# Kernel tuning notes

Hardware: AMD Instinct MI355X
Metric: run time of the kernel (lower is better)

The kernel has to match this reference:

```python
import jax, jax.numpy as jnp
import numpy as np

B, T, DIM, H = 2, 2048, 1024, 16
HD = DIM // H


def setup_inputs() -> dict:
    key = jax.random.key(0)
    k1, k2, k3 = jax.random.split(key, 3)
    std = 1.0 / np.sqrt(DIM)
    x = jax.random.normal(k1, (B, T, DIM), dtype=jnp.float32)
    # torch Linear(dim, 3*dim).weight is [3*dim, dim]; we store the transposed
    # [dim, 3*dim] layout so forward is x @ W_qkv (same math).
    W_qkv = jax.random.uniform(k2, (DIM, 3 * DIM), dtype=jnp.float32, minval=-std, maxval=std)
    W_proj = jax.random.uniform(k3, (DIM, DIM), dtype=jnp.float32, minval=-std, maxval=std)
    return {"x": x, "W_qkv": W_qkv, "W_proj": W_proj}


def reference(x, W_qkv, W_proj):
    Bv, Tv, C = x.shape
    # qkv projection -> [B, T, 3, H, HD] -> q,k,v each [B, H, T, HD]
    qkv = (x @ W_qkv).reshape(Bv, Tv, 3, H, HD)
    qkv = jnp.transpose(qkv, (2, 0, 3, 1, 4))
    q, k, v = qkv[0], qkv[1], qkv[2]
    scale = jnp.asarray(np.sqrt(HD), dtype=x.dtype)
    scores = jnp.einsum('bhqd,bhkd->bhqk', q, k) / scale
    causal = jnp.tril(jnp.ones((Tv, Tv), dtype=bool))  # [T, T]
    scores = jnp.where(causal[None, None, :, :], scores, -jnp.inf)
    attn = jax.nn.softmax(scores, axis=-1)  # [B, H, T, T]
    # entropy per query position, averaged over heads -> [B, T]
    entropy = -(attn * jnp.log(attn + 1e-9)).sum(axis=-1).mean(axis=1)
    # dropout is identity in eval mode
    out = jnp.einsum('bhqk,bhkd->bhqd', attn, v)
    out = jnp.transpose(out, (0, 2, 1, 3)).reshape(Bv, Tv, C)
    return out @ W_proj, entropy
```

## Files before the change

### kernel.cpp

```cpp
#include <hip/hip_runtime.h>


typedef unsigned short u16;
typedef __attribute__((ext_vector_type(8))) __bf16 bf16x8;
typedef __attribute__((ext_vector_type(4))) float float4v;

#define BQ 2
#define TQ 2048
#define DIMQ 1024
#define HQ 16
#define HDQ 64

__device__ __forceinline__ float4v mfma16(bf16x8 a, bf16x8 b, float4v c) {
    return __builtin_amdgcn_mfma_f32_16x16x32_bf16(a, b, c, 0, 0, 0);
}

__device__ __forceinline__ u16 f2bf(float f) {
    unsigned x = __float_as_uint(f);
    return (u16)((x + 0x7FFFu + ((x >> 16) & 1u)) >> 16);
}

__device__ __forceinline__ uint4 cvt8(float4 a, float4 b) {
    union { uint4 v; u16 u[8]; } r;
    r.u[0] = f2bf(a.x); r.u[1] = f2bf(a.y); r.u[2] = f2bf(a.z); r.u[3] = f2bf(a.w);
    r.u[4] = f2bf(b.x); r.u[5] = f2bf(b.y); r.u[6] = f2bf(b.z); r.u[7] = f2bf(b.w);
    return r.v;
}

__device__ __forceinline__ void async16(const u16* g, u16* l) {
    __builtin_amdgcn_global_load_lds(
        (const __attribute__((address_space(1))) void*)g,
        (__attribute__((address_space(3))) void*)l, 16, 0, 0);
}

__device__ __forceinline__ void plswap(unsigned& a, unsigned& b) {
    asm("v_permlane32_swap_b32 %0, %1" : "+v"(a), "+v"(b));
    asm("v_permlane16_swap_b32 %0, %1" : "+v"(a), "+v"(b));
}

__device__ __forceinline__ void tr_tile(
    const float* __restrict__ in, u16* __restrict__ out, int R, int C,
    int tx, int ty, int tid, float (*T)[68])
{
    const int k0 = ty * 64, n0 = tx * 64;
    {
        int r = tid >> 2, cc = (tid & 3) << 4;
        const float* src = in + (size_t)(k0 + r) * C + n0 + cc;
        float4 v0 = ((const float4*)src)[0];
        float4 v1 = ((const float4*)src)[1];
        float4 v2 = ((const float4*)src)[2];
        float4 v3 = ((const float4*)src)[3];
        *(float4*)&T[r][cc + 0]  = v0;
        *(float4*)&T[r][cc + 4]  = v1;
        *(float4*)&T[r][cc + 8]  = v2;
        *(float4*)&T[r][cc + 12] = v3;
    }
    __syncthreads();
    {
        int nr = tid >> 2, kc = (tid & 3) << 4;
        union { uint4 v; u16 u[8]; } o0, o1;
#pragma unroll
        for (int j = 0; j < 8; ++j) o0.u[j] = f2bf(T[kc + j][nr]);
#pragma unroll
        for (int j = 0; j < 8; ++j) o1.u[j] = f2bf(T[kc + 8 + j][nr]);
        u16* dst = out + (size_t)(n0 + nr) * R + k0 + kc;
        ((uint4*)dst)[0] = o0.v;
        *(uint4*)(dst + 8) = o1.v;
    }
}

__global__ __launch_bounds__(256) void prep_kernel(
    const float* __restrict__ x, const float* __restrict__ Wq,
    const float* __restrict__ Wp,
    u16* __restrict__ xb, u16* __restrict__ Wt, u16* __restrict__ Wpt)
{
    __shared__ float T[64][68];
    const int bx = blockIdx.x, tid = threadIdx.x;
    if (bx < 2048) {
        int i = (bx * 256 + tid) * 8;
        float4 a = *(const float4*)(x + i);
        float4 b = *(const float4*)(x + i + 4);
        *(uint4*)(xb + i) = cvt8(a, b);
    } else if (bx < 2816) {
        int bb = bx - 2048;
        tr_tile(Wq, Wt, DIMQ, 3 * DIMQ, bb % 48, bb / 48, tid, T);
    } else {
        int bb = bx - 2816;
        tr_tile(Wp, Wpt, DIMQ, DIMQ, bb & 15, bb >> 4, tid, T);
    }
}

__global__ __launch_bounds__(256) void tr_cvt(
    const float* __restrict__ in, u16* __restrict__ out, int R, int C)
{
    __shared__ float T[64][68];
    tr_tile(in, out, R, C, blockIdx.x, blockIdx.y, threadIdx.x, T);
}

template <int TILEM, int MODE>
__global__ __launch_bounds__(256) void gemm_db(
    const u16* __restrict__ A, const u16* __restrict__ Bt,
    int M, int N, int K,
    u16* __restrict__ Qo, u16* __restrict__ Ko, u16* __restrict__ Vt,
    float* __restrict__ Of, const float* __restrict__ EntIn)
{
    constexpr int MT = TILEM / 32;
    constexpr int AR = TILEM / 64;
    __shared__ u16 As[2][TILEM * 32];
    __shared__ u16 Bs[2][128 * 32];

    const int tid = threadIdx.x;
    const int nbn = gridDim.x;
    const int flat = blockIdx.y * nbn + blockIdx.x;
    const int cpx = (nbn * gridDim.y) >> 3;
    const int swz = (flat & 7) * cpx + (flat >> 3);
    const int bm = swz / nbn, bn = swz % nbn;
    const int wave = tid >> 6, lane = tid & 63;
    const int quad = lane >> 4, c = lane & 15;
    const int wm = wave >> 1, wn = wave & 1;
    const int x3 = c & 3;

    const float4v z = {0.f, 0.f, 0.f, 0.f};
    float4v acc[MT][4];
#pragma unroll
    for (int mt = 0; mt < MT; ++mt)
#pragma unroll
        for (int tn = 0; tn < 4; ++tn) acc[mt][tn] = z;

    const int srow = tid >> 2;
    const int schunk8 = (((tid & 3) ^ (srow & 3)) << 3);
    const u16* ga = A  + (size_t)(bm * TILEM + srow) * K + schunk8;
    const u16* gb = Bt + (size_t)(bn * 128  + srow) * K + schunk8;

#pragma unroll
    for (int p = 0; p < AR; ++p)
        async16(ga + (size_t)(p * 64) * K, As[0] + p * 2048 + tid * 8);
#pragma unroll
    for (int p = 0; p < 2; ++p)
        async16(gb + (size_t)(p * 64) * K, Bs[0] + p * 2048 + tid * 8);

    const int niter = K >> 5;
    for (int it = 0; it < niter; ++it) {
        __syncthreads();
        if (it + 1 < niter) {
            const int nb = (it + 1) & 1;
            const int kc = (it + 1) * 32;
#pragma unroll
            for (int p = 0; p < AR; ++p)
                async16(ga + kc + (size_t)(p * 64) * K, As[nb] + p * 2048 + tid * 8);
#pragma unroll
            for (int p = 0; p < 2; ++p)
                async16(gb + kc + (size_t)(p * 64) * K, Bs[nb] + p * 2048 + tid * 8);
        }
        const u16* as = As[it & 1];
        const u16* bs = Bs[it & 1];

        bf16x8 af[MT], bfr[4];
#pragma unroll
        for (int mt = 0; mt < MT; ++mt)
            af[mt] = *(const bf16x8*)&as[(wm * (TILEM / 2) + mt * 16 + c) * 32 +
                                         ((quad ^ x3) << 3)];
#pragma unroll
        for (int tn = 0; tn < 4; ++tn)
            bfr[tn] = *(const bf16x8*)&bs[(wn * 64 + tn * 16 + c) * 32 +
                                          ((quad ^ x3) << 3)];
#pragma unroll
        for (int mt = 0; mt < MT; ++mt)
#pragma unroll
            for (int tn = 0; tn < 4; ++tn)
                acc[mt][tn] = mfma16(af[mt], bfr[tn], acc[mt][tn]);
    }

#pragma unroll
    for (int mt = 0; mt < MT; ++mt)
#pragma unroll
        for (int tn = 0; tn < 4; ++tn) {
            int gm0 = bm * TILEM + wm * (TILEM / 2) + mt * 16 + quad * 4;
            int gn  = bn * 128 + wn * 64 + tn * 16 + c;
            if (MODE == 0) {
                int s = gn >> 10, h = (gn >> 6) & 15, d = gn & 63;
                int b = gm0 >> 11, t0 = gm0 & 2047;
                size_t bh = (size_t)(b * HQ + h);
                if (s == 2) {
                    union { unsigned long long w; u16 u[4]; } pk;
#pragma unroll
                    for (int r = 0; r < 4; ++r) pk.u[r] = f2bf(acc[mt][tn][r]);
                    *(unsigned long long*)&Vt[(bh * HDQ + d) * TQ + t0] = pk.w;
                } else {
                    u16* dst = (s == 0) ? Qo : Ko;
                    float sc = (s == 0) ? 0.18033688f : 1.0f;
#pragma unroll
                    for (int r = 0; r < 4; ++r)
                        dst[(bh * TQ + t0 + r) * HDQ + d] = f2bf(acc[mt][tn][r] * sc);
                }
            } else {
#pragma unroll
                for (int r = 0; r < 4; ++r)
                    Of[(size_t)(gm0 + r) * N + gn] = acc[mt][tn][r];
            }
        }

    if (MODE == 1 && bn == 0 && bm < 16) {
        int i = bm * 256 + tid;
        int b = i >> 11, t = i & 2047;
        float s = 0.f;
#pragma unroll
        for (int h = 0; h < HQ; ++h) s += EntIn[((size_t)(b * HQ + h)) * TQ + t];
        Of[(size_t)BQ * TQ * DIMQ + i] = s * (1.0f / HQ);
    }
}

__global__ __launch_bounds__(256) void attn_kernel(
    const u16* __restrict__ Q, const u16* __restrict__ K,
    const u16* __restrict__ Vt, u16* __restrict__ AO,
    float* __restrict__ Ent)
{
    const int d = blockIdx.x;
    const int j = d >> 3;
    const int bh = (d & 7) * 4 + (j >> 4);
    int pt = j & 15;
    if (j & 32) pt = 15 - pt;
    const int qt[2] = { pt, 31 - pt };

    const int tid = threadIdx.x;
    const int wave = tid >> 6, lane = tid & 63;
    const int kw = wave & 1;
    const int qh = wave >> 1;
    const int quad = lane >> 4, c = lane & 15;
    const int x7 = c & 7;

    __shared__ u16 Ks[2][64 * 64];
    __shared__ u16 Vs[2][64 * 64];
    __shared__ float Red[2][64][64];
    __shared__ float lred[2][2][2][16], tred[2][2][2][16];

    const u16* Qp = Q  + (size_t)bh * TQ * HDQ;
    const u16* Kp = K  + (size_t)bh * TQ * HDQ;
    const u16* Vp = Vt + (size_t)bh * HDQ * TQ;

    const int qb[2] = { qt[0] * 64 + qh * 32, qt[1] * 64 + qh * 32 };

    bf16x8 qf[2][2][2];
#pragma unroll
    for (int s = 0; s < 2; ++s)
#pragma unroll
        for (int qs = 0; qs < 2; ++qs) {
            const u16* qr = Qp + (size_t)(qb[s] + qs * 16 + c) * HDQ;
            qf[s][qs][0] = *(const bf16x8*)(qr + quad * 8);
            qf[s][qs][1] = *(const bf16x8*)(qr + 32 + quad * 8);
        }

    const float MX2 = 17.312336f;
    const float4v z = {0.f, 0.f, 0.f, 0.f};
    const float4v mz = {-MX2, -MX2, -MX2, -MX2};
    float4v oacc[2][2][4];
#pragma unroll
    for (int s = 0; s < 2; ++s)
#pragma unroll
        for (int qs = 0; qs < 2; ++qs)
#pragma unroll
            for (int tn = 0; tn < 4; ++tn) oacc[s][qs][tn] = z;
    float lp[2][2] = {{0.f,0.f},{0.f,0.f}}, tp[2][2] = {{0.f,0.f},{0.f,0.f}};

    const int ntile = qt[1] + 1;

    const int srow = tid >> 3;
    const int schunk8 = (((tid & 7) ^ (srow & 7)) << 3);
    const u16* ka = Kp + (size_t)srow * HDQ + schunk8;
    const u16* va = Vp + (size_t)srow * TQ + schunk8;

    {
        async16(ka, Ks[0] + tid * 8);
        async16(ka + (size_t)32 * HDQ, Ks[0] + 2048 + tid * 8);
        async16(va, Vs[0] + tid * 8);
        async16(va + (size_t)32 * TQ, Vs[0] + 2048 + tid * 8);
    }

    for (int jt = 0; jt < ntile; ++jt) {
        __syncthreads();
        if (jt + 1 < ntile) {
            int nb = (jt + 1) & 1;
            async16(ka + (size_t)((jt + 1) * 64) * HDQ, Ks[nb] + tid * 8);
            async16(ka + (size_t)((jt + 1) * 64 + 32) * HDQ, Ks[nb] + 2048 + tid * 8);
            async16(va + (jt + 1) * 64, Vs[nb] + tid * 8);
            async16(va + (size_t)32 * TQ + (jt + 1) * 64, Vs[nb] + 2048 + tid * 8);
        }
        const u16* ksb = Ks[jt & 1];
        const u16* vsb = Vs[jt & 1];

        bf16x8 kf[2][2], vf[4];
#pragma unroll
        for (int kt = 0; kt < 2; ++kt) {
            int base = (kw * 32 + kt * 16 + c) * 64;
            kf[kt][0] = *(const bf16x8*)&ksb[base + ((quad ^ x7) << 3)];
            kf[kt][1] = *(const bf16x8*)&ksb[base + (((quad + 4) ^ x7) << 3)];
        }
#pragma unroll
        for (int tn = 0; tn < 4; ++tn)
            vf[tn] = *(const bf16x8*)&vsb[(tn * 16 + c) * 64 +
                                          (((kw * 4 + quad) ^ x7) << 3)];

#pragma unroll
        for (int s = 0; s < 2; ++s) {
            if (s == 0 && jt > qt[0]) continue;
#pragma unroll
            for (int qs = 0; qs < 2; ++qs) {
                unsigned w0[2], w1[2];
#pragma unroll
                for (int kt = 0; kt < 2; ++kt) {
                    float4v sacc = mz;
                    sacc = mfma16(kf[kt][0], qf[s][qs][0], sacc);
                    sacc = mfma16(kf[kt][1], qf[s][qs][1], sacc);
                    if (jt == qt[s]) {
#pragma unroll
                        for (int r = 0; r < 4; ++r) {
                            int kg = jt * 64 + kw * 32 + kt * 16 + quad * 4 + r;
                            if (kg > qb[s] + qs * 16 + c) sacc[r] = -1e30f;
                        }
                    }
                    float pv[4];
#pragma unroll
                    for (int r = 0; r < 4; ++r) {
                        float sv = sacc[r];
                        float p;
                        asm("v_exp_f32 %0, %1" : "=v"(p) : "v"(sv));
                        lp[s][qs] += p;
                        tp[s][qs] += p * sv;
                        pv[r] = p;
                    }
                    asm("v_cvt_pk_bf16_f32 %0, %1, %2"
                        : "=v"(w0[kt]) : "v"(pv[0]), "v"(pv[1]));
                    asm("v_cvt_pk_bf16_f32 %0, %1, %2"
                        : "=v"(w1[kt]) : "v"(pv[2]), "v"(pv[3]));
                }
                plswap(w0[0], w0[1]);
                plswap(w1[0], w1[1]);
                union { uint4 u; bf16x8 v; } P;
                P.u = (uint4){w0[0], w1[0], w0[1], w1[1]};
                __builtin_amdgcn_s_setprio(1);
#pragma unroll
                for (int tn = 0; tn < 4; ++tn)
                    oacc[s][qs][tn] = mfma16(vf[tn], P.v, oacc[s][qs][tn]);
                __builtin_amdgcn_s_setprio(0);
            }
        }
    }

    __syncthreads();
#pragma unroll
    for (int s = 0; s < 2; ++s)
#pragma unroll
        for (int qs = 0; qs < 2; ++qs) {
            lp[s][qs] += __shfl_xor(lp[s][qs], 16);
            lp[s][qs] += __shfl_xor(lp[s][qs], 32);
            tp[s][qs] += __shfl_xor(tp[s][qs], 16);
            tp[s][qs] += __shfl_xor(tp[s][qs], 32);
        }

    if (kw == 1) {
#pragma unroll
        for (int s = 0; s < 2; ++s)
#pragma unroll
            for (int qs = 0; qs < 2; ++qs) {
#pragma unroll
                for (int tn = 0; tn < 4; ++tn)
#pragma unroll
                    for (int r = 0; r < 4; ++r)
                        Red[qh][((s * 2 + qs) * 4 + tn) * 4 + r][lane] =
                            oacc[s][qs][tn][r];
                if (quad == 0) {
                    lred[qh][s][qs][c] = lp[s][qs];
                    tred[qh][s][qs][c] = tp[s][qs];
                }
            }
    }
    __syncthreads();
    if (kw == 0) {
        const int b = bh >> 4, h = bh & 15;
#pragma unroll
        for (int s = 0; s < 2; ++s)
#pragma unroll
            for (int qs = 0; qs < 2; ++qs) {
#pragma unroll
                for (int tn = 0; tn < 4; ++tn)
#pragma unroll
                    for (int r = 0; r < 4; ++r)
                        oacc[s][qs][tn][r] +=
                            Red[qh][((s * 2 + qs) * 4 + tn) * 4 + r][lane];
                float l = lp[s][qs] + lred[qh][s][qs][c];
                float t = tp[s][qs] + tred[qh][s][qs][c];

                float inv = 1.0f / l;
                u16* dst = AO + ((size_t)(b * TQ + qb[s] + qs * 16 + c)) * DIMQ
                           + h * HDQ;
#pragma unroll
                for (int tn = 0; tn < 4; ++tn) {
                    unsigned u[4];
#pragma unroll
                    for (int r = 0; r < 4; ++r)
                        u[r] = (unsigned)f2bf(oacc[s][qs][tn][r] * inv);
                    uint2 pk;
                    pk.x = u[0] | (u[1] << 16);
                    pk.y = u[2] | (u[3] << 16);
                    *(uint2*)(dst + tn * 16 + quad * 4) = pk;
                }
                if (quad == 0)
                    Ent[(size_t)bh * TQ + qb[s] + qs * 16 + c] =
                        __logf(l) - 0.69314718f * t / l;
            }
    }
}

extern "C" void kernel_launch(void* const* d_in, const int* in_sizes, int n_in,
                              void* d_out, int out_size, void* d_ws, size_t ws_size,
                              hipStream_t stream) {
    const float* x     = (const float*)d_in[0];
    const float* Wqkv  = (const float*)d_in[1];
    const float* Wproj = (const float*)d_in[2];
    float* out = (float*)d_out;

    const size_t NE = (size_t)BQ * HQ * TQ * HDQ;
    const size_t WQN = (size_t)3 * DIMQ * DIMQ;
    const size_t WPN = (size_t)DIMQ * DIMQ;
    u16* Qb  = (u16*)d_ws;
    u16* Kb  = Qb + NE;
    u16* Vtb = Kb + NE;
    u16* xb  = Vtb + NE;
    u16* Wt  = xb + NE;
    u16* AO  = xb;

    const size_t need = (4 * NE + WQN + WPN) * 2 + (size_t)BQ * HQ * TQ * 4;
    const bool room = ws_size >= need;
    u16* Wpt = room ? (Wt + WQN) : Wt;
    float* Ent = room ? (float*)(Wpt + WPN) : (float*)(Wt + WQN);

    prep_kernel<<<dim3(room ? 3072 : 2816), 256, 0, stream>>>(
        x, Wqkv, Wproj, xb, Wt, Wpt);
    gemm_db<128, 0><<<dim3(24, 32), 256, 0, stream>>>(
        xb, Wt, BQ * TQ, 3 * DIMQ, DIMQ, Qb, Kb, Vtb, nullptr, nullptr);
    if (!room)
        tr_cvt<<<dim3(16, 16), 256, 0, stream>>>(Wproj, Wpt, DIMQ, DIMQ);
    attn_kernel<<<dim3(512), 256, 0, stream>>>(Qb, Kb, Vtb, AO, Ent);
    gemm_db<64, 1><<<dim3(8, 64), 256, 0, stream>>>(
        AO, Wpt, BQ * TQ, DIMQ, DIMQ, nullptr, nullptr, nullptr, out, Ent);
}
```

Baseline: 177.9 us.

## Double attention block to 512 threads with one 16-row query slice per wave

The attention kernel now uses 8 waves per block, with each wave handling a single 16-row query slice instead of two, halving per-wave accumulator and Q-fragment registers. The block's shared memory is consolidated into one K/V double buffer, which is reused for the cross-wave output reduction, so the block needs less shared memory. Launch bounds request 512 threads with 4 blocks per CU to raise occupancy. In exchange, each K/V fragment read from shared memory is amortized over fewer MFMAs, and the register cap may force spills.

Result: faster. 168.2 us, median of 3 (-5.5%).

```diff
diff --git a/kernel.cpp b/kernel.cpp
--- a/kernel.cpp
+++ b/kernel.cpp
@@ -210,7 +210,7 @@
     }
 }
 
-__global__ __launch_bounds__(256) void attn_kernel(
+__global__ __launch_bounds__(512, 4) void attn_kernel(
     const u16* __restrict__ Q, const u16* __restrict__ K,
     const u16* __restrict__ Vt, u16* __restrict__ AO,
     float* __restrict__ Ent)
@@ -229,38 +229,32 @@
     const int quad = lane >> 4, c = lane & 15;
     const int x7 = c & 7;
 
-    __shared__ u16 Ks[2][64 * 64];
-    __shared__ u16 Vs[2][64 * 64];
-    __shared__ float Red[2][64][64];
-    __shared__ float lred[2][2][2][16], tred[2][2][2][16];
+    __shared__ u16 Sbuf[4][64 * 64];
+    __shared__ float lred[4][2][16], tred[4][2][16];
 
     const u16* Qp = Q  + (size_t)bh * TQ * HDQ;
     const u16* Kp = K  + (size_t)bh * TQ * HDQ;
     const u16* Vp = Vt + (size_t)bh * HDQ * TQ;
 
-    const int qb[2] = { qt[0] * 64 + qh * 32, qt[1] * 64 + qh * 32 };
-
-    bf16x8 qf[2][2][2];
-#pragma unroll
-    for (int s = 0; s < 2; ++s)
-#pragma unroll
-        for (int qs = 0; qs < 2; ++qs) {
-            const u16* qr = Qp + (size_t)(qb[s] + qs * 16 + c) * HDQ;
-            qf[s][qs][0] = *(const bf16x8*)(qr + quad * 8);
-            qf[s][qs][1] = *(const bf16x8*)(qr + 32 + quad * 8);
-        }
+    const int qb[2] = { qt[0] * 64 + qh * 16, qt[1] * 64 + qh * 16 };
+
+    bf16x8 qf[2][2];
+#pragma unroll
+    for (int s = 0; s < 2; ++s) {
+        const u16* qr = Qp + (size_t)(qb[s] + c) * HDQ;
+        qf[s][0] = *(const bf16x8*)(qr + quad * 8);
+        qf[s][1] = *(const bf16x8*)(qr + 32 + quad * 8);
+    }
 
     const float MX2 = 17.312336f;
     const float4v z = {0.f, 0.f, 0.f, 0.f};
     const float4v mz = {-MX2, -MX2, -MX2, -MX2};
-    float4v oacc[2][2][4];
+    float4v oacc[2][4];
 #pragma unroll
     for (int s = 0; s < 2; ++s)
 #pragma unroll
-        for (int qs = 0; qs < 2; ++qs)
-#pragma unroll
-            for (int tn = 0; tn < 4; ++tn) oacc[s][qs][tn] = z;
-    float lp[2][2] = {{0.f,0.f},{0.f,0.f}}, tp[2][2] = {{0.f,0.f},{0.f,0.f}};
+        for (int tn = 0; tn < 4; ++tn) oacc[s][tn] = z;
+    float lp[2] = {0.f, 0.f}, tp[2] = {0.f, 0.f};
 
     const int ntile = qt[1] + 1;
 
@@ -270,23 +264,19 @@
     const u16* va = Vp + (size_t)srow * TQ + schunk8;
 
     {
-        async16(ka, Ks[0] + tid * 8);
-        async16(ka + (size_t)32 * HDQ, Ks[0] + 2048 + tid * 8);
-        async16(va, Vs[0] + tid * 8);
-        async16(va + (size_t)32 * TQ, Vs[0] + 2048 + tid * 8);
+        async16(ka, Sbuf[0] + tid * 8);
+        async16(va, Sbuf[2] + tid * 8);
     }
 
     for (int jt = 0; jt < ntile; ++jt) {
         __syncthreads();
         if (jt + 1 < ntile) {
             int nb = (jt + 1) & 1;
-            async16(ka + (size_t)((jt + 1) * 64) * HDQ, Ks[nb] + tid * 8);
-            async16(ka + (size_t)((jt + 1) * 64 + 32) * HDQ, Ks[nb] + 2048 + tid * 8);
-            async16(va + (jt + 1) * 64, Vs[nb] + tid * 8);
-            async16(va + (size_t)32 * TQ + (jt + 1) * 64, Vs[nb] + 2048 + tid * 8);
-        }
-        const u16* ksb = Ks[jt & 1];
-        const u16* vsb = Vs[jt & 1];
+            async16(ka + (size_t)((jt + 1) * 64) * HDQ, Sbuf[nb] + tid * 8);
+            async16(va + (jt + 1) * 64, Sbuf[2 + nb] + tid * 8);
+        }
+        const u16* ksb = Sbuf[jt & 1];
+        const u16* vsb = Sbuf[2 + (jt & 1)];
 
         bf16x8 kf[2][2], vf[4];
 #pragma unroll
@@ -303,111 +293,100 @@
 #pragma unroll
         for (int s = 0; s < 2; ++s) {
             if (s == 0 && jt > qt[0]) continue;
-#pragma unroll
-            for (int qs = 0; qs < 2; ++qs) {
-                unsigned w0[2], w1[2];
-#pragma unroll
-                for (int kt = 0; kt < 2; ++kt) {
-                    float4v sacc = mz;
-                    sacc = mfma16(kf[kt][0], qf[s][qs][0], sacc);
-                    sacc = mfma16(kf[kt][1], qf[s][qs][1], sacc);
-                    if (jt == qt[s]) {
-#pragma unroll
-                        for (int r = 0; r < 4; ++r) {
-                            int kg = jt * 64 + kw * 32 + kt * 16 + quad * 4 + r;
-                            if (kg > qb[s] + qs * 16 + c) sacc[r] = -1e30f;
-                        }
+            unsigned w0[2], w1[2];
+#pragma unroll
+            for (int kt = 0; kt < 2; ++kt) {
+                float4v sacc = mz;
+                sacc = mfma16(kf[kt][0], qf[s][0], sacc);
+                sacc = mfma16(kf[kt][1], qf[s][1], sacc);
+                if (jt == qt[s]) {
+#pragma unroll
+                    for (int r = 0; r < 4; ++r) {
+                        int kg = jt * 64 + kw * 32 + kt * 16 + quad * 4 + r;
+                        if (kg > qb[s] + c) sacc[r] = -1e30f;
                     }
-                    float pv[4];
-#pragma unroll
-                    for (int r = 0; r < 4; ++r) {
-                        float sv = sacc[r];
-                        float p;
-                        asm("v_exp_f32 %0, %1" : "=v"(p) : "v"(sv));
-                        lp[s][qs] += p;
-                        tp[s][qs] += p * sv;
-                        pv[r] = p;
-                    }
-                    asm("v_cvt_pk_bf16_f32 %0, %1, %2"
-                        : "=v"(w0[kt]) : "v"(pv[0]), "v"(pv[1]));
-                    asm("v_cvt_pk_bf16_f32 %0, %1, %2"
-                        : "=v"(w1[kt]) : "v"(pv[2]), "v"(pv[3]));
                 }
-                plswap(w0[0], w0[1]);
-                plswap(w1[0], w1[1]);
-                union { uint4 u; bf16x8 v; } P;
-                P.u = (uint4){w0[0], w1[0], w0[1], w1[1]};
-                __builtin_amdgcn_s_setprio(1);
-#pragma unroll
-                for (int tn = 0; tn < 4; ++tn)
-                    oacc[s][qs][tn] = mfma16(vf[tn], P.v, oacc[s][qs][tn]);
-                __builtin_amdgcn_s_setprio(0);
+                float pv[4];
+#pragma unroll
+                for (int r = 0; r < 4; ++r) {
+                    float sv = sacc[r];
+                    float p;
+                    asm("v_exp_f32 %0, %1" : "=v"(p) : "v"(sv));
+                    lp[s] += p;
+                    tp[s] += p * sv;
+                    pv[r] = p;
+                }
+                asm("v_cvt_pk_bf16_f32 %0, %1, %2"
+                    : "=v"(w0[kt]) : "v"(pv[0]), "v"(pv[1]));
+                asm("v_cvt_pk_bf16_f32 %0, %1, %2"
+                    : "=v"(w1[kt]) : "v"(pv[2]), "v"(pv[3]));
             }
-        }
-    }
-
+            plswap(w0[0], w0[1]);
+            plswap(w1[0], w1[1]);
+            union { uint4 u; bf16x8 v; } P;
+            P.u = (uint4){w0[0], w1[0], w0[1], w1[1]};
+            __builtin_amdgcn_s_setprio(1);
+#pragma unroll
+            for (int tn = 0; tn < 4; ++tn)
+                oacc[s][tn] = mfma16(vf[tn], P.v, oacc[s][tn]);
+            __builtin_amdgcn_s_setprio(0);
+        }
+    }
+
+#pragma unroll
+    for (int s = 0; s < 2; ++s) {
+        lp[s] += __shfl_xor(lp[s], 16); lp[s] += __shfl_xor(lp[s], 32);
+        tp[s] += __shfl_xor(tp[s], 16); tp[s] += __shfl_xor(tp[s], 32);
+    }
     __syncthreads();
-#pragma unroll
-    for (int s = 0; s < 2; ++s)
-#pragma unroll
-        for (int qs = 0; qs < 2; ++qs) {
-            lp[s][qs] += __shfl_xor(lp[s][qs], 16);
-            lp[s][qs] += __shfl_xor(lp[s][qs], 32);
-            tp[s][qs] += __shfl_xor(tp[s][qs], 16);
-            tp[s][qs] += __shfl_xor(tp[s][qs], 32);
-        }
-
+
+    float* Red = (float*)&Sbuf[0][0];
     if (kw == 1) {
 #pragma unroll
-        for (int s = 0; s < 2; ++s)
-#pragma unroll
-            for (int qs = 0; qs < 2; ++qs) {
-#pragma unroll
-                for (int tn = 0; tn < 4; ++tn)
-#pragma unroll
-                    for (int r = 0; r < 4; ++r)
-                        Red[qh][((s * 2 + qs) * 4 + tn) * 4 + r][lane] =
-                            oacc[s][qs][tn][r];
-                if (quad == 0) {
-                    lred[qh][s][qs][c] = lp[s][qs];
-                    tred[qh][s][qs][c] = tp[s][qs];
-                }
+        for (int s = 0; s < 2; ++s) {
+#pragma unroll
+            for (int tn = 0; tn < 4; ++tn)
+#pragma unroll
+                for (int r = 0; r < 4; ++r)
+                    Red[((qh * 32) + (s * 4 + tn) * 4 + r) * 64 + lane] =
+                        oacc[s][tn][r];
+            if (quad == 0) {
+                lred[qh][s][c] = lp[s];
+                tred[qh][s][c] = tp[s];
             }
+        }
     }
     __syncthreads();
     if (kw == 0) {
         const int b = bh >> 4, h = bh & 15;
 #pragma unroll
-        for (int s = 0; s < 2; ++s)
-#pragma unroll
-            for (int qs = 0; qs < 2; ++qs) {
-#pragma unroll
-                for (int tn = 0; tn < 4; ++tn)
-#pragma unroll
-                    for (int r = 0; r < 4; ++r)
-                        oacc[s][qs][tn][r] +=
-                            Red[qh][((s * 2 + qs) * 4 + tn) * 4 + r][lane];
-                float l = lp[s][qs] + lred[qh][s][qs][c];
-                float t = tp[s][qs] + tred[qh][s][qs][c];
-
-                float inv = 1.0f / l;
-                u16* dst = AO + ((size_t)(b * TQ + qb[s] + qs * 16 + c)) * DIMQ
-                           + h * HDQ;
-#pragma unroll
-                for (int tn = 0; tn < 4; ++tn) {
-                    unsigned u[4];
-#pragma unroll
-                    for (int r = 0; r < 4; ++r)
-                        u[r] = (unsigned)f2bf(oacc[s][qs][tn][r] * inv);
-                    uint2 pk;
-                    pk.x = u[0] | (u[1] << 16);
-                    pk.y = u[2] | (u[3] << 16);
-                    *(uint2*)(dst + tn * 16 + quad * 4) = pk;
-                }
-                if (quad == 0)
-                    Ent[(size_t)bh * TQ + qb[s] + qs * 16 + c] =
-                        __logf(l) - 0.69314718f * t / l;
+        for (int s = 0; s < 2; ++s) {
+#pragma unroll
+            for (int tn = 0; tn < 4; ++tn)
+#pragma unroll
+                for (int r = 0; r < 4; ++r)
+                    oacc[s][tn][r] +=
+                        Red[((qh * 32) + (s * 4 + tn) * 4 + r) * 64 + lane];
+            float l = lp[s] + lred[qh][s][c];
+            float t = tp[s] + tred[qh][s][c];
+
+            float inv = 1.0f / l;
+            u16* dst = AO + ((size_t)(b * TQ + qb[s] + c)) * DIMQ + h * HDQ;
+#pragma unroll
+            for (int tn = 0; tn < 4; ++tn) {
+                unsigned u[4];
+#pragma unroll
+                for (int r = 0; r < 4; ++r)
+                    u[r] = (unsigned)f2bf(oacc[s][tn][r] * inv);
+                uint2 pk;
+                pk.x = u[0] | (u[1] << 16);
+                pk.y = u[2] | (u[3] << 16);
+                *(uint2*)(dst + tn * 16 + quad * 4) = pk;
             }
+            if (quad == 0)
+                Ent[(size_t)bh * TQ + qb[s] + c] =
+                    __logf(l) - 0.69314718f * t / l;
+        }
     }
 }
 
@@ -440,7 +419,7 @@
         xb, Wt, BQ * TQ, 3 * DIMQ, DIMQ, Qb, Kb, Vtb, nullptr, nullptr);
     if (!room)
         tr_cvt<<<dim3(16, 16), 256, 0, stream>>>(Wproj, Wpt, DIMQ, DIMQ);
-    attn_kernel<<<dim3(512), 256, 0, stream>>>(Qb, Kb, Vtb, AO, Ent);
+    attn_kernel<<<dim3(512), 512, 0, stream>>>(Qb, Kb, Vtb, AO, Ent);
     gemm_db<64, 1><<<dim3(8, 64), 256, 0, stream>>>(
         AO, Wpt, BQ * TQ, DIMQ, DIMQ, nullptr, nullptr, nullptr, out, Ent);
 }
```
